# Kernel optimization log

Measured on AMD Instinct MI355X. Metric: run time of the kernel, lower is better.

The kernel has to match this reference:

```python
import jax, jax.numpy as jnp
import numpy as np

H, C, PQ, PV = 12, 16, 4, 8  # heads, scalar head dim, query points, value points
EPS = 1e-8


def setup_inputs() -> dict:
    key = jax.random.key(0)
    ks = jax.random.split(key, 16)
    B, N, S, Z = 2, 512, 384, 128
    def w(k, fan_in, shape):
        return jax.random.normal(k, shape, jnp.float32) / np.sqrt(fan_in)
    return {
        's': jax.random.normal(ks[0], (B, N, S), jnp.float32),
        'z': jax.random.normal(ks[1], (B, N, N, Z), jnp.float32),
        'R': jax.random.normal(ks[2], (B, N, 3, 3), jnp.float32),
        't': jax.random.normal(ks[3], (B, N, 3), jnp.float32),
        'Wq': w(ks[4], S, (S, H * C)),
        'Wk': w(ks[5], S, (S, H * C)),
        'Wv': w(ks[6], S, (S, H * C)),
        'Wqp': w(ks[7], S, (S, H * PQ * 3)),
        'Wkp': w(ks[8], S, (S, H * PQ * 3)),
        'Wvp': w(ks[9], S, (S, H * PV * 3)),
        'Wb': w(ks[10], Z, (Z, H)),
        'head_weights': jax.random.normal(ks[11], (H,), jnp.float32) * 0.1,
        'Wout': w(ks[12], H * (C + 4 * PV + Z), (H * (C + 4 * PV + Z), S)),
    }


def reference(s, z, R, t, Wq, Wk, Wv, Wqp, Wkp, Wvp, Wb, head_weights, Wout):
    B, N, _ = s.shape
    Zc = z.shape[-1]
    # scalar q/k/v: [B,N,H,C]
    q = (s @ Wq).reshape(B, N, H, C)
    k = (s @ Wk).reshape(B, N, H, C)
    v = (s @ Wv).reshape(B, N, H, C)
    # point q/k/v in local frames, then map to global: x_g = R x + t
    def to_global(Wp, P):
        p = (s @ Wp).reshape(B, N, H, P, 3)
        return jnp.einsum('bnxy,bnhpy->bnhpx', R, p) + t[:, :, None, None, :]
    qp = to_global(Wqp, PQ)   # [B,N,H,PQ,3]
    kp = to_global(Wkp, PQ)
    vp = to_global(Wvp, PV)   # [B,N,H,PV,3]
    # pair bias [B,H,N,N]
    b = jnp.einsum('bijz,zh->bhij', z, Wb)
    # scalar attention logits
    scal = jnp.einsum('bihc,bjhc->bhij', q, k) / np.sqrt(C)
    # squared point distances via expansion (avoid [B,N,N,H,PQ,3] tensor)
    qq = jnp.sum(qp * qp, axis=(-1, -2))                    # [B,N,H]
    kk = jnp.sum(kp * kp, axis=(-1, -2))                    # [B,N,H]
    qk = jnp.einsum('bihpx,bjhpx->bhij', qp, kp)
    dist2 = qq.transpose(0, 2, 1)[:, :, :, None] + kk.transpose(0, 2, 1)[:, :, None, :] - 2.0 * qk
    gamma = jax.nn.softplus(head_weights)                   # [H]
    wC = np.sqrt(2.0 / (9.0 * PQ))
    wL = np.sqrt(1.0 / 3.0)
    logits = wL * (scal + b) - (wL * wC / 2.0) * gamma[None, :, None, None] * dist2
    a = jax.nn.softmax(logits, axis=-1)                     # [B,H,N,N]
    # scalar output
    o = jnp.einsum('bhij,bjhc->bihc', a, v).reshape(B, N, H * C)
    # point output: aggregate in global frame, then back to local: R^T (x - t)
    opt_g = jnp.einsum('bhij,bjhpx->bihpx', a, vp)
    d = opt_g - t[:, :, None, None, :]
    opt = jnp.einsum('bnyx,bnhpy->bnhpx', R, d)             # R^T d
    opt_norm = jnp.sqrt(jnp.sum(opt * opt, axis=-1) + EPS)  # [B,N,H,PV]
    # pair output
    opair = jnp.einsum('bhij,bijz->bihz', a, z).reshape(B, N, H * Zc)
    cat = jnp.concatenate([o, opt.reshape(B, N, H * PV * 3),
                           opt_norm.reshape(B, N, H * PV), opair], axis=-1)
    return cat @ Wout
```

## Files before the change

kernel.cpp:

```cpp
#include <hip/hip_runtime.h>
#include <math.h>

#define BB 2
#define NN 512
#define SDIM 384
#define ZDIM 128
#define HH 12
#define CDIM 16
#define PQ 4
#define PV 8
#define BN (BB*NN)
#define CATD 2112

#define WL  0.57735026918962576f
#define LAM 0.06804138174397717f

#define OFF_Q    0
#define OFF_QP   196608
#define OFF_QQ   344064
#define OFF_KT4  356352
#define OFF_KPT4 552960
#define OFF_KKT  700416
#define OFF_V    712704
#define OFF_VP   909312
#define OFF_CAT  7495680

__device__ __forceinline__ float dot4(float4 a, float4 b) {
    return a.x*b.x + a.y*b.y + a.z*b.z + a.w*b.w;
}
__device__ __forceinline__ void fma4(float4& a, float s, float4 b) {
    a.x += s*b.x; a.y += s*b.y; a.z += s*b.z; a.w += s*b.w;
}
__device__ __forceinline__ void add4(float4& a, float4 b) {
    a.x += b.x; a.y += b.y; a.z += b.z; a.w += b.w;
}
__device__ __forceinline__ void mul4(float4& a, float s) {
    a.x *= s; a.y *= s; a.z *= s; a.w *= s;
}

__global__ __launch_bounds__(256) void k_proj(
    const float* __restrict__ s, const float* __restrict__ Rg, const float* __restrict__ tg,
    const float* __restrict__ Wq, const float* __restrict__ Wk, const float* __restrict__ Wv,
    const float* __restrict__ Wqp, const float* __restrict__ Wkp, const float* __restrict__ Wvp,
    float* __restrict__ ws)
{
    __shared__ float4 pL4[2][144];
    __shared__ float  sqL[2][96];
    __shared__ float  Rt[2][12];
    const int t = threadIdx.x;
    const int n0 = blockIdx.x * 2;
    const int b  = n0 >> 9;
    const int nloc = n0 & 511;

    if (t < 24) {
        int rr = t / 12, c = t % 12;
        Rt[rr][c] = (c < 9) ? Rg[(n0+rr)*9 + c] : tg[(n0+rr)*3 + (c-9)];
    }
    const float* s0 = s + (size_t)n0*SDIM;
    const float* s1 = s0 + SDIM;
    __syncthreads();

    float4* Q4g  = (float4*)(ws + OFF_Q);
    float4* V4g  = (float4*)(ws + OFF_V);
    float4* KT4g = (float4*)(ws + OFF_KT4);

    for (int it = 0; it < 2; ++it) {
        int g = t + it*256;
        if (g >= 288) break;
        const float4* W4; int wc4, ld4, dst;
        if (g < 48)       { W4 = (const float4*)Wq;  wc4 = g;     ld4 = 48; dst = 0; }
        else if (g < 96)  { W4 = (const float4*)Wk;  wc4 = g-48;  ld4 = 48; dst = 1; }
        else if (g < 144) { W4 = (const float4*)Wv;  wc4 = g-96;  ld4 = 48; dst = 2; }
        else if (g < 180) { W4 = (const float4*)Wqp; wc4 = g-144; ld4 = 36; dst = 3; }
        else if (g < 216) { W4 = (const float4*)Wkp; wc4 = g-180; ld4 = 36; dst = 4; }
        else              { W4 = (const float4*)Wvp; wc4 = g-216; ld4 = 72; dst = 5; }
        float4 acc0 = {0,0,0,0}, acc1 = {0,0,0,0};
        #pragma unroll 4
        for (int r = 0; r < SDIM; ++r) {
            float4 wv = W4[r*ld4 + wc4];
            float f0 = s0[r], f1 = s1[r];
            fma4(acc0, f0, wv);
            fma4(acc1, f1, wv);
        }
        if (dst == 0) {
            Q4g[(size_t)n0*48 + wc4] = acc0;
            Q4g[(size_t)(n0+1)*48 + wc4] = acc1;
        } else if (dst == 1) {
            size_t base = ((size_t)(b*48 + wc4))*512 + nloc;
            KT4g[base] = acc0; KT4g[base+1] = acc1;
        } else if (dst == 2) {
            V4g[(size_t)n0*48 + wc4] = acc0;
            V4g[(size_t)(n0+1)*48 + wc4] = acc1;
        } else if (dst == 3) {
            pL4[0][wc4] = acc0; pL4[1][wc4] = acc1;
        } else if (dst == 4) {
            pL4[0][36+wc4] = acc0; pL4[1][36+wc4] = acc1;
        } else {
            pL4[0][72+wc4] = acc0; pL4[1][72+wc4] = acc1;
        }
    }
    __syncthreads();

    for (int task = t; task < 384; task += 256) {
        int rr = task / 192, pt = task % 192;
        const float* pl = (const float*)pL4[rr];
        int off = (pt < 48) ? pt*3 : (pt < 96 ? 144 + (pt-48)*3 : 288 + (pt-96)*3);
        float p0 = pl[off], p1 = pl[off+1], p2 = pl[off+2];
        const float* R = Rt[rr];
        float g0 = R[0]*p0 + R[1]*p1 + R[2]*p2 + R[9];
        float g1 = R[3]*p0 + R[4]*p1 + R[5]*p2 + R[10];
        float g2 = R[6]*p0 + R[7]*p1 + R[8]*p2 + R[11];
        int bn = n0 + rr, n = bn & 511;
        if (pt < 48) {
            int o = pt*3;
            float* d = ws + OFF_QP + (size_t)bn*144 + o;
            d[0] = g0; d[1] = g1; d[2] = g2;
            sqL[rr][pt] = g0*g0 + g1*g1 + g2*g2;
        } else if (pt < 96) {
            int pc = (pt-48)*3;
            float gg[3] = {g0,g1,g2};
            #pragma unroll
            for (int x = 0; x < 3; ++x) {
                int pcx = pc + x;
                ws[OFF_KPT4 + (((size_t)(b*36 + (pcx>>2)))*512 + n)*4 + (pcx&3)] = gg[x];
            }
            sqL[rr][pt] = g0*g0 + g1*g1 + g2*g2;
        } else {
            int o = (pt-96)*3;
            float* d = ws + OFF_VP + (size_t)bn*288 + o;
            d[0] = g0; d[1] = g1; d[2] = g2;
        }
    }
    __syncthreads();

    if (t < 48) {
        int rr = t / 24, u = t % 24;
        int bn = n0 + rr, n = bn & 511;
        if (u < 12) {
            float sm = sqL[rr][u*4] + sqL[rr][u*4+1] + sqL[rr][u*4+2] + sqL[rr][u*4+3];
            ws[OFF_QQ + (size_t)bn*12 + u] = sm;
        } else {
            int h = u - 12;
            float sm = sqL[rr][48+h*4] + sqL[rr][48+h*4+1] + sqL[rr][48+h*4+2] + sqL[rr][48+h*4+3];
            ws[OFF_KKT + ((size_t)(b*12 + h))*512 + n] = sm;
        }
    }
}

__global__ __launch_bounds__(512, 2) void k_attn(
    const float* __restrict__ z, const float* __restrict__ Rg, const float* __restrict__ tg,
    const float* __restrict__ hw, const float* __restrict__ Wb, float* __restrict__ ws)
{
    __shared__ __align__(16) float aL[HH*516];
    __shared__ float4 optgS4[72];
    __shared__ float RiL[9], tiL[3], sInv[12];

    const int t = threadIdx.x;
    const int d = blockIdx.x;
    const int xcd = d & 7, slot = d >> 3;
    const int bi = (xcd < 4) ? (xcd*128 + slot) : (512 + (xcd-4)*128 + slot);
    const int b = bi >> 9;

    if (t < 9)             RiL[t]   = Rg[bi*9 + t];
    if (t >= 9 && t < 12)  tiL[t-9] = tg[bi*3 + (t-9)];

    float gam[HH];
    #pragma unroll
    for (int h = 0; h < HH; ++h) {
        float x = hw[h];
        gam[h] = (x > 20.f) ? x : log1pf(__expf(x));
    }

    {
        const int j = t;
        float pb[HH];
        #pragma unroll
        for (int h = 0; h < HH; ++h) pb[h] = 0.f;
        const float4* zrow4 = (const float4*)z + ((size_t)bi*512 + j)*32;
        #pragma unroll 4
        for (int c4 = 0; c4 < 32; ++c4) {
            const float4 zq = zrow4[c4];
            const float* wb = Wb + c4*48;
            #pragma unroll
            for (int e = 0; e < 4; ++e) {
                const float zv = ((const float*)&zq)[e];
                const float* w = wb + e*12;
                #pragma unroll
                for (int h = 0; h < HH; ++h) pb[h] += zv * w[h];
            }
        }
        const float4* Q4u  = (const float4*)(ws + OFF_Q  + (size_t)bi*192);
        const float4* QP4u = (const float4*)(ws + OFF_QP + (size_t)bi*144);
        const float*  QQu  = ws + OFF_QQ + (size_t)bi*12;
        const float4* KT4  = (const float4*)(ws + OFF_KT4)  + (size_t)b*48*512;
        const float4* KPT4 = (const float4*)(ws + OFF_KPT4) + (size_t)b*36*512;
        const float*  KKT  = ws + OFF_KKT  + (size_t)b*12*512;
        for (int h = 0; h < HH; ++h) {
            float scal = 0.f, qk = 0.f;
            #pragma unroll
            for (int cg = 0; cg < 4; ++cg)
                scal += dot4(Q4u[h*4+cg], KT4[(h*4+cg)*512 + j]);
            #pragma unroll
            for (int pg = 0; pg < 3; ++pg)
                qk += dot4(QP4u[h*3+pg], KPT4[(h*3+pg)*512 + j]);
            float dist2 = QQu[h] + KKT[h*512 + j] - 2.f*qk;
            aL[h*516 + j] = WL*(scal*0.25f + pb[h]) - LAM*gam[h]*dist2;
        }
    }
    __syncthreads();

    {
        const int w = t >> 6, lane = t & 63;
        for (int h = w; h < HH; h += 8) {
            float* row = aL + h*516;
            float m = -1e30f;
            #pragma unroll
            for (int k = 0; k < 8; ++k) m = fmaxf(m, row[lane + 64*k]);
            #pragma unroll
            for (int off = 32; off > 0; off >>= 1) m = fmaxf(m, __shfl_xor(m, off));
            float ssum = 0.f;
            #pragma unroll
            for (int k = 0; k < 8; ++k) {
                float e = __expf(row[lane + 64*k] - m);
                row[lane + 64*k] = e;
                ssum += e;
            }
            #pragma unroll
            for (int off = 32; off > 0; off >>= 1) ssum += __shfl_xor(ssum, off);
            if (lane == 0) sInv[h] = 1.f / ssum;
        }
    }
    __syncthreads();

    float4 acc0 = {0,0,0,0}, acc1 = {0,0,0,0}, acc2 = {0,0,0,0};
    int rid = -1, seg = 0;

#define FMA8(ZB, AP0, AP1, AP2, JT) do { \
    float4 av0 = *(const float4*)((AP0) + (JT)); \
    float4 av1 = *(const float4*)((AP1) + (JT)); \
    float4 av2 = *(const float4*)((AP2) + (JT)); \
    float4 aw0 = *(const float4*)((AP0) + (JT) + 4); \
    float4 aw1 = *(const float4*)((AP1) + (JT) + 4); \
    float4 aw2 = *(const float4*)((AP2) + (JT) + 4); \
    fma4(acc0, av0.x, ZB[0]); fma4(acc1, av1.x, ZB[0]); fma4(acc2, av2.x, ZB[0]); \
    fma4(acc0, av0.y, ZB[1]); fma4(acc1, av1.y, ZB[1]); fma4(acc2, av2.y, ZB[1]); \
    fma4(acc0, av0.z, ZB[2]); fma4(acc1, av1.z, ZB[2]); fma4(acc2, av2.z, ZB[2]); \
    fma4(acc0, av0.w, ZB[3]); fma4(acc1, av1.w, ZB[3]); fma4(acc2, av2.w, ZB[3]); \
    fma4(acc0, aw0.x, ZB[4]); fma4(acc1, aw1.x, ZB[4]); fma4(acc2, aw2.x, ZB[4]); \
    fma4(acc0, aw0.y, ZB[5]); fma4(acc1, aw1.y, ZB[5]); fma4(acc2, aw2.y, ZB[5]); \
    fma4(acc0, aw0.z, ZB[6]); fma4(acc1, aw1.z, ZB[6]); fma4(acc2, aw2.z, ZB[6]); \
    fma4(acc0, aw0.w, ZB[7]); fma4(acc1, aw1.w, ZB[7]); fma4(acc2, aw2.w, ZB[7]); \
} while (0)

    if (t < 384) {
        seg = t >> 7;
        rid = t & 127;
        const int hg = rid >> 5, zc4 = rid & 31;
        const int j0 = seg*176;
        const int ngrp = (seg == 2) ? 20 : 22;
        const float4* Zp = (const float4*)z + (size_t)bi*512*32 + zc4;
        const float* a0p = aL + hg*516;
        const float* a1p = aL + (hg+4)*516;
        const float* a2p = aL + (hg+8)*516;
        float4 zA[8], zB[8];
        #pragma unroll
        for (int e = 0; e < 8; ++e) zA[e] = Zp[(size_t)(j0+e)*32];
        for (int p = 0; p < ngrp; p += 2) {
            const int jt = j0 + p*8;
            #pragma unroll
            for (int e = 0; e < 8; ++e) zB[e] = Zp[(size_t)(jt+8+e)*32];
            FMA8(zA, a0p, a1p, a2p, jt);
            if (p + 2 < ngrp) {
                #pragma unroll
                for (int e = 0; e < 8; ++e) zA[e] = Zp[(size_t)(jt+16+e)*32];
            }
            FMA8(zB, a0p, a1p, a2p, jt + 8);
        }
    } else if (t < 504) {
        const int v = t - 384;
        seg = v / 40;
        const int w = v % 40;
        rid = 128 + w;
        const int j0 = seg*176, j1 = (seg == 2) ? 512 : j0 + 176;
        const float4* P; int S, D, O, hg;
        if (w < 16) {
            hg = w >> 2; S = 48; D = 16; O = hg*4 + (w & 3);
            P = (const float4*)(ws + OFF_V) + (size_t)b*512*48;
        } else {
            const int v2 = w - 16;
            hg = v2 / 6; S = 72; D = 24; O = hg*6 + v2 % 6;
            P = (const float4*)(ws + OFF_VP) + (size_t)b*512*72;
        }
        const float* a0p = aL + hg*516;
        const float* a1p = aL + (hg+4)*516;
        const float* a2p = aL + (hg+8)*516;
        #pragma unroll 2
        for (int jt = j0; jt < j1; jt += 4) {
            float4 av0 = *(const float4*)(a0p + jt);
            float4 av1 = *(const float4*)(a1p + jt);
            float4 av2 = *(const float4*)(a2p + jt);
            #pragma unroll
            for (int e = 0; e < 4; ++e) {
                const size_t base = (size_t)(jt+e)*S + O;
                fma4(acc0, ((const float*)&av0)[e], P[base]);
                fma4(acc1, ((const float*)&av1)[e], P[base + D]);
                fma4(acc2, ((const float*)&av2)[e], P[base + 2*D]);
            }
        }
    }
    __syncthreads();
    float4* sc4 = (float4*)aL;
    if (rid >= 0) {
        const int si = (seg*168 + rid)*3;
        sc4[si] = acc0; sc4[si+1] = acc1; sc4[si+2] = acc2;
    }
    __syncthreads();

    if (t < 168) {
        float4 r0 = {0,0,0,0}, r1 = {0,0,0,0}, r2 = {0,0,0,0};
        #pragma unroll
        for (int ss = 0; ss < 3; ++ss) {
            const int si = (ss*168 + t)*3;
            add4(r0, sc4[si]); add4(r1, sc4[si+1]); add4(r2, sc4[si+2]);
        }
        int typ, hg;
        if (t < 128)      { typ = 0; hg = t >> 5; }
        else if (t < 144) { typ = 1; hg = (t-128) >> 2; }
        else              { typ = 2; hg = (t-144) / 6; }
        mul4(r0, sInv[hg]); mul4(r1, sInv[hg+4]); mul4(r2, sInv[hg+8]);
        float4* cat4 = (float4*)(ws + OFF_CAT);
        const size_t cb = (size_t)bi * 528;
        if (typ == 0) {
            const int zc4 = t & 31;
            cat4[cb + 144 + (hg  )*32 + zc4] = r0;
            cat4[cb + 144 + (hg+4)*32 + zc4] = r1;
            cat4[cb + 144 + (hg+8)*32 + zc4] = r2;
        } else if (typ == 1) {
            const int c4 = (t-128) & 3;
            cat4[cb + (hg  )*4 + c4] = r0;
            cat4[cb + (hg+4)*4 + c4] = r1;
            cat4[cb + (hg+8)*4 + c4] = r2;
        } else {
            const int po = (t-144) % 6;
            optgS4[(hg  )*6 + po] = r0;
            optgS4[(hg+4)*6 + po] = r1;
            optgS4[(hg+8)*6 + po] = r2;
        }
    }
    __syncthreads();

    if (t < 96) {
        const float* og = (const float*)optgS4;
        int h = t >> 3, p = t & 7;
        int o = h*24 + p*3;
        float d0 = og[o]   - tiL[0];
        float d1 = og[o+1] - tiL[1];
        float d2 = og[o+2] - tiL[2];
        float ox = RiL[0]*d0 + RiL[3]*d1 + RiL[6]*d2;
        float oy = RiL[1]*d0 + RiL[4]*d1 + RiL[7]*d2;
        float oz = RiL[2]*d0 + RiL[5]*d1 + RiL[8]*d2;
        float* cat = ws + OFF_CAT + (size_t)bi*CATD;
        cat[192 + o]     = ox;
        cat[192 + o + 1] = oy;
        cat[192 + o + 2] = oz;
        cat[480 + h*8 + p] = sqrtf(ox*ox + oy*oy + oz*oz + 1e-8f);
    }
}

__global__ __launch_bounds__(384) void k_out(
    const float* __restrict__ Wout, const float* __restrict__ ws, float* __restrict__ out)
{
    const int t = threadIdx.x;
    const int row0 = blockIdx.x * 4;
    const float* c0 = ws + OFF_CAT + (size_t)(row0+0)*CATD;
    const float* c1 = c0 + CATD;
    const float* c2 = c1 + CATD;
    const float* c3 = c2 + CATD;
    float a0 = 0.f, a1 = 0.f, a2 = 0.f, a3 = 0.f;
    #pragma unroll 8
    for (int r = 0; r < CATD; ++r) {
        float w = Wout[(size_t)r*384 + t];
        a0 += c0[r]*w; a1 += c1[r]*w; a2 += c2[r]*w; a3 += c3[r]*w;
    }
    out[(size_t)(row0+0)*384 + t] = a0;
    out[(size_t)(row0+1)*384 + t] = a1;
    out[(size_t)(row0+2)*384 + t] = a2;
    out[(size_t)(row0+3)*384 + t] = a3;
}

extern "C" void kernel_launch(void* const* d_in, const int* in_sizes, int n_in,
                              void* d_out, int out_size, void* d_ws, size_t ws_size,
                              hipStream_t stream)
{
    const float* s    = (const float*)d_in[0];
    const float* z    = (const float*)d_in[1];
    const float* R    = (const float*)d_in[2];
    const float* tt   = (const float*)d_in[3];
    const float* Wq   = (const float*)d_in[4];
    const float* Wk   = (const float*)d_in[5];
    const float* Wv   = (const float*)d_in[6];
    const float* Wqp  = (const float*)d_in[7];
    const float* Wkp  = (const float*)d_in[8];
    const float* Wvp  = (const float*)d_in[9];
    const float* Wb   = (const float*)d_in[10];
    const float* hw   = (const float*)d_in[11];
    const float* Wout = (const float*)d_in[12];
    float* ws  = (float*)d_ws;
    float* out = (float*)d_out;

    hipLaunchKernelGGL(k_proj, dim3(BN/2), dim3(256), 0, stream,
                       s, R, tt, Wq, Wk, Wv, Wqp, Wkp, Wvp, ws);
    hipLaunchKernelGGL(k_attn, dim3(BN),   dim3(512), 0, stream, z, R, tt, hw, Wb, ws);
    hipLaunchKernelGGL(k_out,  dim3(BN/4), dim3(384), 0, stream, Wout, ws, out);
}
```

Before: 739.9 us.

## Split attention into logits/softmax and accumulation kernels; widen output GEMM rows

The fused attention kernel is split in two. k_logits computes the pair bias and logits in registers, does a block-wide softmax through cross-warp shared reductions, and writes normalized probabilities to a global workspace. k_acc reloads those probabilities into LDS and does the weighted aggregation over z, v and vp, so the per-head LDS softmax pass and final rescale are dropped. This adds a global round trip of the probability matrix, an extra launch, and a second full read of z, since both kernels read it. The output projection now handles 8 rows per block instead of 4, reusing each Wout load across more rows.

```diff
diff --git a/kernel.cpp b/kernel.cpp
--- a/kernel.cpp
+++ b/kernel.cpp
@@ -23,6 +23,7 @@
 #define OFF_KKT  700416
 #define OFF_V    712704
 #define OFF_VP   909312
+#define OFF_P    1204224
 #define OFF_CAT  7495680
 
 __device__ __forceinline__ float dot4(float4 a, float4 b) {
@@ -33,9 +34,6 @@
 }
 __device__ __forceinline__ void add4(float4& a, float4 b) {
     a.x += b.x; a.y += b.y; a.z += b.z; a.w += b.w;
-}
-__device__ __forceinline__ void mul4(float4& a, float s) {
-    a.x *= s; a.y *= s; a.z *= s; a.w *= s;
 }
 
 __global__ __launch_bounds__(256) void k_proj(
@@ -147,48 +145,45 @@
     }
 }
 
-__global__ __launch_bounds__(512, 2) void k_attn(
-    const float* __restrict__ z, const float* __restrict__ Rg, const float* __restrict__ tg,
-    const float* __restrict__ hw, const float* __restrict__ Wb, float* __restrict__ ws)
+__global__ __launch_bounds__(512, 2) void k_logits(
+    const float* __restrict__ z, const float* __restrict__ hw,
+    const float* __restrict__ Wb, float* __restrict__ ws)
 {
-    __shared__ __align__(16) float aL[HH*516];
-    __shared__ float4 optgS4[72];
-    __shared__ float RiL[9], tiL[3], sInv[12];
+    __shared__ float gamS[12];
+    __shared__ float wred[8][12];
+    __shared__ float gred[12];
 
     const int t = threadIdx.x;
     const int d = blockIdx.x;
     const int xcd = d & 7, slot = d >> 3;
     const int bi = (xcd < 4) ? (xcd*128 + slot) : (512 + (xcd-4)*128 + slot);
     const int b = bi >> 9;
-
-    if (t < 9)             RiL[t]   = Rg[bi*9 + t];
-    if (t >= 9 && t < 12)  tiL[t-9] = tg[bi*3 + (t-9)];
-
-    float gam[HH];
+    const int j = t;
+
+    if (t < 12) {
+        float x = hw[t];
+        gamS[t] = (x > 20.f) ? x : log1pf(__expf(x));
+    }
+    __syncthreads();
+
+    float pb[HH];
     #pragma unroll
-    for (int h = 0; h < HH; ++h) {
-        float x = hw[h];
-        gam[h] = (x > 20.f) ? x : log1pf(__expf(x));
+    for (int h = 0; h < HH; ++h) pb[h] = 0.f;
+    const float4* zrow4 = (const float4*)z + ((size_t)bi*512 + j)*32;
+    #pragma unroll 4
+    for (int c4 = 0; c4 < 32; ++c4) {
+        const float4 zq = zrow4[c4];
+        const float* wb = Wb + c4*48;
+        #pragma unroll
+        for (int e = 0; e < 4; ++e) {
+            const float zv = ((const float*)&zq)[e];
+            const float* w = wb + e*12;
+            #pragma unroll
+            for (int h = 0; h < HH; ++h) pb[h] += zv * w[h];
+        }
     }
 
     {
-        const int j = t;
-        float pb[HH];
-        #pragma unroll
-        for (int h = 0; h < HH; ++h) pb[h] = 0.f;
-        const float4* zrow4 = (const float4*)z + ((size_t)bi*512 + j)*32;
-        #pragma unroll 4
-        for (int c4 = 0; c4 < 32; ++c4) {
-            const float4 zq = zrow4[c4];
-            const float* wb = Wb + c4*48;
-            #pragma unroll
-            for (int e = 0; e < 4; ++e) {
-                const float zv = ((const float*)&zq)[e];
-                const float* w = wb + e*12;
-                #pragma unroll
-                for (int h = 0; h < HH; ++h) pb[h] += zv * w[h];
-            }
-        }
         const float4* Q4u  = (const float4*)(ws + OFF_Q  + (size_t)bi*192);
         const float4* QP4u = (const float4*)(ws + OFF_QP + (size_t)bi*144);
         const float*  QQu  = ws + OFF_QQ + (size_t)bi*12;
@@ -204,31 +199,71 @@
             for (int pg = 0; pg < 3; ++pg)
                 qk += dot4(QP4u[h*3+pg], KPT4[(h*3+pg)*512 + j]);
             float dist2 = QQu[h] + KKT[h*512 + j] - 2.f*qk;
-            aL[h*516 + j] = WL*(scal*0.25f + pb[h]) - LAM*gam[h]*dist2;
-        }
-    }
-    __syncthreads();
+            pb[h] = WL*(scal*0.25f + pb[h]) - LAM*gamS[h]*dist2;
+        }
+    }
+
+    const int w = t >> 6, lane = t & 63;
+    #pragma unroll
+    for (int h = 0; h < HH; ++h) {
+        float m = pb[h];
+        #pragma unroll
+        for (int off = 32; off > 0; off >>= 1) m = fmaxf(m, __shfl_xor(m, off));
+        if (lane == 0) wred[w][h] = m;
+    }
+    __syncthreads();
+    if (t < 12) {
+        float m = wred[0][t];
+        #pragma unroll
+        for (int ww = 1; ww < 8; ++ww) m = fmaxf(m, wred[ww][t]);
+        gred[t] = m;
+    }
+    __syncthreads();
+    #pragma unroll
+    for (int h = 0; h < HH; ++h) {
+        float e = __expf(pb[h] - gred[h]);
+        pb[h] = e;
+        #pragma unroll
+        for (int off = 32; off > 0; off >>= 1) e += __shfl_xor(e, off);
+        if (lane == 0) wred[w][h] = e;
+    }
+    __syncthreads();
+    if (t < 12) {
+        float ssum = 0.f;
+        #pragma unroll
+        for (int ww = 0; ww < 8; ++ww) ssum += wred[ww][t];
+        gred[t] = 1.f / ssum;
+    }
+    __syncthreads();
+
+    float* Pg = ws + OFF_P + (size_t)bi*HH*512;
+    #pragma unroll
+    for (int h = 0; h < HH; ++h)
+        Pg[h*512 + j] = pb[h] * gred[h];
+}
+
+__global__ __launch_bounds__(512, 2) void k_acc(
+    const float* __restrict__ z, const float* __restrict__ Rg, const float* __restrict__ tg,
+    float* __restrict__ ws)
+{
+    __shared__ __align__(16) float aL[HH*516];
+    __shared__ float4 optgS4[72];
+    __shared__ float RiL[9], tiL[3];
+
+    const int t = threadIdx.x;
+    const int d = blockIdx.x;
+    const int xcd = d & 7, slot = d >> 3;
+    const int bi = (xcd < 4) ? (xcd*128 + slot) : (512 + (xcd-4)*128 + slot);
+    const int b = bi >> 9;
+
+    if (t < 9)             RiL[t]   = Rg[bi*9 + t];
+    if (t >= 9 && t < 12)  tiL[t-9] = tg[bi*3 + (t-9)];
 
     {
-        const int w = t >> 6, lane = t & 63;
-        for (int h = w; h < HH; h += 8) {
-            float* row = aL + h*516;
-            float m = -1e30f;
-            #pragma unroll
-            for (int k = 0; k < 8; ++k) m = fmaxf(m, row[lane + 64*k]);
-            #pragma unroll
-            for (int off = 32; off > 0; off >>= 1) m = fmaxf(m, __shfl_xor(m, off));
-            float ssum = 0.f;
-            #pragma unroll
-            for (int k = 0; k < 8; ++k) {
-                float e = __expf(row[lane + 64*k] - m);
-                row[lane + 64*k] = e;
-                ssum += e;
-            }
-            #pragma unroll
-            for (int off = 32; off > 0; off >>= 1) ssum += __shfl_xor(ssum, off);
-            if (lane == 0) sInv[h] = 1.f / ssum;
-        }
+        const float* Pg = ws + OFF_P + (size_t)bi*HH*512;
+        #pragma unroll
+        for (int i = t; i < HH*512; i += 512)
+            aL[(i >> 9)*516 + (i & 511)] = Pg[i];
     }
     __syncthreads();
 
@@ -327,7 +362,6 @@
         if (t < 128)      { typ = 0; hg = t >> 5; }
         else if (t < 144) { typ = 1; hg = (t-128) >> 2; }
         else              { typ = 2; hg = (t-144) / 6; }
-        mul4(r0, sInv[hg]); mul4(r1, sInv[hg+4]); mul4(r2, sInv[hg+8]);
         float4* cat4 = (float4*)(ws + OFF_CAT);
         const size_t cb = (size_t)bi * 528;
         if (typ == 0) {
@@ -371,21 +405,29 @@
     const float* __restrict__ Wout, const float* __restrict__ ws, float* __restrict__ out)
 {
     const int t = threadIdx.x;
-    const int row0 = blockIdx.x * 4;
-    const float* c0 = ws + OFF_CAT + (size_t)(row0+0)*CATD;
-    const float* c1 = c0 + CATD;
-    const float* c2 = c1 + CATD;
-    const float* c3 = c2 + CATD;
-    float a0 = 0.f, a1 = 0.f, a2 = 0.f, a3 = 0.f;
-    #pragma unroll 8
+    const int row0 = blockIdx.x * 8;
+    const float* c0 = ws + OFF_CAT + (size_t)row0*CATD;
+    float a0=0.f,a1=0.f,a2=0.f,a3=0.f,a4=0.f,a5=0.f,a6=0.f,a7=0.f;
+    #pragma unroll 16
     for (int r = 0; r < CATD; ++r) {
         float w = Wout[(size_t)r*384 + t];
-        a0 += c0[r]*w; a1 += c1[r]*w; a2 += c2[r]*w; a3 += c3[r]*w;
+        a0 += c0[r]*w;
+        a1 += c0[r +   CATD]*w;
+        a2 += c0[r + 2*CATD]*w;
+        a3 += c0[r + 3*CATD]*w;
+        a4 += c0[r + 4*CATD]*w;
+        a5 += c0[r + 5*CATD]*w;
+        a6 += c0[r + 6*CATD]*w;
+        a7 += c0[r + 7*CATD]*w;
     }
     out[(size_t)(row0+0)*384 + t] = a0;
     out[(size_t)(row0+1)*384 + t] = a1;
     out[(size_t)(row0+2)*384 + t] = a2;
     out[(size_t)(row0+3)*384 + t] = a3;
+    out[(size_t)(row0+4)*384 + t] = a4;
+    out[(size_t)(row0+5)*384 + t] = a5;
+    out[(size_t)(row0+6)*384 + t] = a6;
+    out[(size_t)(row0+7)*384 + t] = a7;
 }
 
 extern "C" void kernel_launch(void* const* d_in, const int* in_sizes, int n_in,
@@ -408,8 +450,9 @@
     float* ws  = (float*)d_ws;
     float* out = (float*)d_out;
 
-    hipLaunchKernelGGL(k_proj, dim3(BN/2), dim3(256), 0, stream,
+    hipLaunchKernelGGL(k_proj,   dim3(BN/2), dim3(256), 0, stream,
                        s, R, tt, Wq, Wk, Wv, Wqp, Wkp, Wvp, ws);
-    hipLaunchKernelGGL(k_attn, dim3(BN),   dim3(512), 0, stream, z, R, tt, hw, Wb, ws);
-    hipLaunchKernelGGL(k_out,  dim3(BN/4), dim3(384), 0, stream, Wout, ws, out);
-}
+    hipLaunchKernelGGL(k_logits, dim3(BN),   dim3(512), 0, stream, z, hw, Wb, ws);
+    hipLaunchKernelGGL(k_acc,    dim3(BN),   dim3(512), 0, stream, z, R, tt, ws);
+    hipLaunchKernelGGL(k_out,    dim3(BN/8), dim3(384), 0, stream, Wout, ws, out);
+}
```

After: 1.046 ms. 41.4% more time.
